# Performance work log

Measured on AMD Instinct MI355X. Metric: run time of the kernel, lower is better.

The kernel has to match this reference:

```python
import jax, jax.numpy as jnp
import numpy as np

B, S, D, H = 2, 2048, 512, 8
DK = D // H


def setup_inputs() -> dict:
    key = jax.random.key(0)
    ks = jax.random.split(key, 6)
    q = jax.random.normal(ks[0], (B, S, D), dtype=jnp.float32)
    k = jax.random.normal(ks[1], (B, S, D), dtype=jnp.float32)
    v = jax.random.normal(ks[2], (B, S, D), dtype=jnp.float32)
    mask = jax.random.randint(ks[3], (1, 1, S, S), 0, 2, dtype=jnp.int32)
    # nn.Linear weights [out, in]; scaled like torch default init
    Wq = jax.random.normal(ks[4], (D, D), dtype=jnp.float32) / np.sqrt(D)
    Wo = jax.random.normal(ks[5], (D, D), dtype=jnp.float32) / np.sqrt(D)
    return {"q": q, "k": k, "v": v, "mask": mask, "Wq": Wq, "Wo": Wo}


def _split_heads(x):
    # [B,S,D] -> [B,H,S,DK]
    return x.reshape(B, S, H, DK).transpose(0, 2, 1, 3)


def reference(q, k, v, mask, Wq, Wo):
    # NOTE: original module applies Wq to q, k AND v (faithful to source bug)
    query = _split_heads(q @ Wq.T)
    key_ = _split_heads(k @ Wq.T)
    value = _split_heads(v @ Wq.T)
    scores = jnp.einsum("bhqd,bhkd->bhqk", query, key_) / np.sqrt(DK).astype(np.float32)
    # original uses masked_fill_(mask==0, 1e-09) BEFORE softmax (not -inf)
    scores = jnp.where(mask == 0, jnp.float32(1e-9), scores)
    attn = jax.nn.softmax(scores, axis=-1)  # dropout p=0.0 -> identity
    x = jnp.einsum("bhqk,bhkd->bhqd", attn, value)
    x = x.transpose(0, 2, 1, 3).reshape(B, S, D)
    return x @ Wo.T
```

## Files before the change

kernel.cpp:

```cpp
#include <hip/hip_runtime.h>
#include <hip/hip_bf16.h>
#include <stdint.h>

#define S_LEN 2048
#define D_MOD 512
#define N_H   8
#define D_K   64

typedef short v8s __attribute__((ext_vector_type(8)));
typedef short v4s __attribute__((ext_vector_type(4)));
typedef float v4f __attribute__((ext_vector_type(4)));

__device__ __forceinline__ short f2bf(float f) {
  union { float f; unsigned u; } a; a.f = f;
  unsigned u = a.u;
  u += 0x7fffu + ((u >> 16) & 1u);
  return (short)(u >> 16);
}
__device__ __forceinline__ short f2bfh(float f) {
  union { float f; unsigned u; } a; a.f = f;
  return (short)((a.u + 0x8000u) >> 16);
}
__device__ __forceinline__ float bf2f(short s) {
  union { unsigned u; float f; } x;
  x.u = ((unsigned)(unsigned short)s) << 16;
  return x.f;
}

__device__ __forceinline__ v4f mfma16(v8s a, v8s b, v4f c) {
  return __builtin_amdgcn_mfma_f32_16x16x32_bf16(a, b, c, 0, 0, 0);
}
__device__ __forceinline__ v4f mfma16x16(v4s a, v4s b, v4f c) {
  return __builtin_amdgcn_mfma_f32_16x16x16bf16_1k(a, b, c, 0, 0, 0);
}

__global__ __launch_bounds__(256) void proj_kernel(
    const float* __restrict__ q, const float* __restrict__ k,
    const float* __restrict__ v, const float* __restrict__ Wq,
    const float* __restrict__ Wo, const int* __restrict__ mask,
    short* __restrict__ QP, short* __restrict__ KP, short* __restrict__ VT,
    short* __restrict__ Wob, unsigned long long* __restrict__ mp)
{
  const int z = blockIdx.z;
  const int tid = threadIdx.x;
  if (z == 3) {
    int bid = blockIdx.x * 8 + blockIdx.y;
    if (bid < 256) {
      int id = bid * 256 + tid;
      const int4* m4 = (const int4*)(mask + (size_t)id * 64);
      unsigned long long w = 0ull;
#pragma unroll
      for (int j = 0; j < 16; j++) {
        int4 mv = m4[j];
        w |= (unsigned long long)(mv.x != 0) << (j * 4 + 0);
        w |= (unsigned long long)(mv.y != 0) << (j * 4 + 1);
        w |= (unsigned long long)(mv.z != 0) << (j * 4 + 2);
        w |= (unsigned long long)(mv.w != 0) << (j * 4 + 3);
      }
      mp[id] = w;
    } else {
      unsigned off = (bid - 256) * 256 + tid;
      float4 x = ((const float4*)Wo)[off];
      v4s p; p.x = f2bf(x.x); p.y = f2bf(x.y); p.z = f2bf(x.z); p.w = f2bf(x.w);
      ((v4s*)Wob)[off] = p;
    }
    return;
  }
  const float* __restrict__ A = (z == 0) ? q : ((z == 1) ? k : v);
  const int m0 = blockIdx.x * 64, n0 = blockIdx.y * 64;
  const int wave = tid >> 6, lane = tid & 63;
  const int quad = lane >> 4, l15 = lane & 15;
  const int wm = wave >> 1, wn = wave & 1;
  __shared__ short As[64][72];
  __shared__ short Bs[64][72];
  v4f acc[2][2];
#pragma unroll
  for (int i = 0; i < 2; i++)
#pragma unroll
    for (int j = 0; j < 2; j++) acc[i][j] = (v4f){0.f, 0.f, 0.f, 0.f};

  float4 a4[4], b4[4];
#pragma unroll
  for (int i = 0; i < 4; i++) {
    int fi = tid + i * 256, r = fi >> 4, c = (fi & 15) << 2;
    a4[i] = *(const float4*)&A[(m0 + r) * 512 + c];
    b4[i] = *(const float4*)&Wq[(n0 + r) * 512 + c];
  }

  for (int kk = 0; kk < 512; kk += 64) {
    __syncthreads();
#pragma unroll
    for (int i = 0; i < 4; i++) {
      int fi = tid + i * 256, r = fi >> 4, c = (fi & 15) << 2;
      v4s ap; ap.x = f2bf(a4[i].x); ap.y = f2bf(a4[i].y); ap.z = f2bf(a4[i].z); ap.w = f2bf(a4[i].w);
      *(v4s*)&As[r][c] = ap;
      v4s bp; bp.x = f2bf(b4[i].x); bp.y = f2bf(b4[i].y); bp.z = f2bf(b4[i].z); bp.w = f2bf(b4[i].w);
      *(v4s*)&Bs[r][c] = bp;
    }
    __syncthreads();
    if (kk + 64 < 512) {
#pragma unroll
      for (int i = 0; i < 4; i++) {
        int fi = tid + i * 256, r = fi >> 4, c = (fi & 15) << 2;
        a4[i] = *(const float4*)&A[(m0 + r) * 512 + kk + 64 + c];
        b4[i] = *(const float4*)&Wq[(n0 + r) * 512 + kk + 64 + c];
      }
    }
#pragma unroll
    for (int ms = 0; ms < 2; ms++)
#pragma unroll
      for (int ns = 0; ns < 2; ns++)
#pragma unroll
        for (int ks = 0; ks < 2; ks++) {
          union { v8s v; v4s h2[2]; } a, bb;
          a.h2[0]  = *(const v4s*)&As[wm * 32 + ms * 16 + l15][ks * 32 + quad * 8];
          a.h2[1]  = *(const v4s*)&As[wm * 32 + ms * 16 + l15][ks * 32 + quad * 8 + 4];
          bb.h2[0] = *(const v4s*)&Bs[wn * 32 + ns * 16 + l15][ks * 32 + quad * 8];
          bb.h2[1] = *(const v4s*)&Bs[wn * 32 + ns * 16 + l15][ks * 32 + quad * 8 + 4];
          acc[ms][ns] = mfma16(a.v, bb.v, acc[ms][ns]);
        }
  }
#pragma unroll
  for (int ms = 0; ms < 2; ms++)
#pragma unroll
    for (int ns = 0; ns < 2; ns++) {
      int mb = m0 + wm * 32 + ms * 16 + quad * 4;
      int n  = n0 + wn * 32 + ns * 16 + l15;
      int bI = mb >> 11, s = mb & 2047, hh = n >> 6, dk = n & 63;
      if (z == 2) {
        v4s pv;
        pv.x = f2bf(acc[ms][ns][0]); pv.y = f2bf(acc[ms][ns][1]);
        pv.z = f2bf(acc[ms][ns][2]); pv.w = f2bf(acc[ms][ns][3]);
        *(v4s*)&VT[((bI * N_H + hh) * D_K + dk) * S_LEN + s] = pv;
      } else {
        short* dst = (z == 0) ? QP : KP;
#pragma unroll
        for (int r = 0; r < 4; r++)
          dst[((bI * N_H + hh) * S_LEN + (s + r)) * D_K + dk] = f2bf(acc[ms][ns][r]);
      }
    }
}

__global__ __launch_bounds__(512, 4) void attn_kernel(
    const short* __restrict__ QP, const short* __restrict__ KP,
    const short* __restrict__ VT, const unsigned long long* __restrict__ MP,
    short* __restrict__ XB)
{
  const int qt = blockIdx.x;
  const int h = blockIdx.y, b = blockIdx.z;
  const int tid = threadIdx.x;
  const int wave = tid >> 6, lane = tid & 63;
  const int quad = lane >> 4, l15 = lane & 15;
  const short* Qh = QP + ((b * N_H + h) * S_LEN) * D_K;
  const short* Kh = KP + ((b * N_H + h) * S_LEN) * D_K;
  const short* Vh = VT + ((b * N_H + h) * D_K) * S_LEN;

  __shared__ short Ks[2][64][72];
  __shared__ short Vs[2][64][72];

  const int qrow = qt * 128 + wave * 16;
  const int srow = tid >> 3;
  const int sc   = (tid & 7) * 8;

  v8s aQ[2];
#pragma unroll
  for (int ks = 0; ks < 2; ks++)
    aQ[ks] = *(const v8s*)&Qh[(qrow + l15) * D_K + ks * 32 + quad * 8];

  const float C1 = 0.18033688011112042f;
  const float C2 = -11.541560327111707f;
  const v4s ONES4 = {16256, 16256, 16256, 16256};
  v4f accX[4], accL = (v4f){0.f, 0.f, 0.f, 0.f};
#pragma unroll
  for (int u = 0; u < 4; u++) accX[u] = (v4f){0.f, 0.f, 0.f, 0.f};

  v8s kr = *(const v8s*)&Kh[srow * D_K + sc];
  v8s vr = *(const v8s*)&Vh[srow * S_LEN + sc];
  *(v8s*)&Ks[0][srow][sc] = kr;
  *(v8s*)&Vs[0][srow][sc] = vr;
  unsigned long long mwc = MP[(qrow + l15) * 32];
  unsigned long long mwn = 0ull;
  __syncthreads();

  for (int kt = 0; kt < 32; kt++) {
    const int cur = kt & 1;
    if (kt + 1 < 32) {
      const int c1 = (kt + 1) * 64;
      kr = *(const v8s*)&Kh[(c1 + srow) * D_K + sc];
      vr = *(const v8s*)&Vh[srow * S_LEN + c1 + sc];
      mwn = MP[(qrow + l15) * 32 + kt + 1];
    }

    v4s pa[4];
#pragma unroll
    for (int tp = 0; tp < 4; tp++) {
      v8s bK0 = *(const v8s*)&Ks[cur][tp * 16 + l15][quad * 8];
      v8s bK1 = *(const v8s*)&Ks[cur][tp * 16 + l15][32 + quad * 8];
      v4f s = mfma16(bK0, aQ[0], (v4f){0.f, 0.f, 0.f, 0.f});
      s = mfma16(bK1, aQ[1], s);
      unsigned mb = (unsigned)(mwc >> (tp * 16 + quad * 4));
      v4s pk;
#pragma unroll
      for (int r = 0; r < 4; r++) {
        float se = ((mb >> r) & 1u) ? s[r] : 0.0f;
        float p = __builtin_amdgcn_exp2f(fmaf(se, C1, C2));
        pk[r] = f2bfh(p);
      }
      pa[tp] = pk;
    }

#pragma unroll
    for (int u = 0; u < 4; u++) {
      const short* vb_ = &Vs[cur][u * 16 + l15][quad * 4];
#pragma unroll
      for (int tp = 0; tp < 4; tp++) {
        v4s bV = *(const v4s*)&vb_[tp * 16];
        accX[u] = mfma16x16(pa[tp], bV, accX[u]);
      }
    }
#pragma unroll
    for (int tp = 0; tp < 4; tp++)
      accL = mfma16x16(pa[tp], ONES4, accL);

    if (kt + 1 < 32) {
      *(v8s*)&Ks[cur ^ 1][srow][sc] = kr;
      *(v8s*)&Vs[cur ^ 1][srow][sc] = vr;
    }
    __syncthreads();
    mwc = mwn;
  }

  v4f linv;
#pragma unroll
  for (int r = 0; r < 4; r++) linv[r] = 1.0f / accL[r];
#pragma unroll
  for (int u = 0; u < 4; u++)
#pragma unroll
    for (int r = 0; r < 4; r++) {
      int srw = qrow + quad * 4 + r;
      XB[(b * S_LEN + srw) * D_MOD + h * D_K + u * 16 + l15] =
          f2bf(accX[u][r] * linv[r]);
    }
}

__global__ __launch_bounds__(256) void outproj_kernel(
    const short* __restrict__ XB, const short* __restrict__ Wob,
    float* __restrict__ out)
{
  const int m0 = blockIdx.x * 64, n0 = blockIdx.y * 64;
  const int tid = threadIdx.x;
  const int wave = tid >> 6, lane = tid & 63;
  const int quad = lane >> 4, l15 = lane & 15;
  const int wm = wave >> 1, wn = wave & 1;
  __shared__ short As[64][72];
  __shared__ short Bs[64][72];

  v4f acc[2][2];
#pragma unroll
  for (int i = 0; i < 2; i++)
#pragma unroll
    for (int j = 0; j < 2; j++) acc[i][j] = (v4f){0.f, 0.f, 0.f, 0.f};

  v8s a8[2], b8[2];
#pragma unroll
  for (int i = 0; i < 2; i++) {
    int fi = tid + i * 256, r = fi >> 3, c = (fi & 7) << 3;
    a8[i] = *(const v8s*)&XB[(m0 + r) * 512 + c];
    b8[i] = *(const v8s*)&Wob[(n0 + r) * 512 + c];
  }

  for (int kk = 0; kk < 512; kk += 64) {
    __syncthreads();
#pragma unroll
    for (int i = 0; i < 2; i++) {
      int fi = tid + i * 256, r = fi >> 3, c = (fi & 7) << 3;
      *(v8s*)&As[r][c] = a8[i];
      *(v8s*)&Bs[r][c] = b8[i];
    }
    __syncthreads();
    if (kk + 64 < 512) {
#pragma unroll
      for (int i = 0; i < 2; i++) {
        int fi = tid + i * 256, r = fi >> 3, c = (fi & 7) << 3;
        a8[i] = *(const v8s*)&XB[(m0 + r) * 512 + kk + 64 + c];
        b8[i] = *(const v8s*)&Wob[(n0 + r) * 512 + kk + 64 + c];
      }
    }
#pragma unroll
    for (int ms = 0; ms < 2; ms++)
#pragma unroll
      for (int ns = 0; ns < 2; ns++)
#pragma unroll
        for (int ks = 0; ks < 2; ks++) {
          union { v8s v; v4s h2[2]; } a, bb;
          a.h2[0]  = *(const v4s*)&As[wm * 32 + ms * 16 + l15][ks * 32 + quad * 8];
          a.h2[1]  = *(const v4s*)&As[wm * 32 + ms * 16 + l15][ks * 32 + quad * 8 + 4];
          bb.h2[0] = *(const v4s*)&Bs[wn * 32 + ns * 16 + l15][ks * 32 + quad * 8];
          bb.h2[1] = *(const v4s*)&Bs[wn * 32 + ns * 16 + l15][ks * 32 + quad * 8 + 4];
          acc[ms][ns] = mfma16(a.v, bb.v, acc[ms][ns]);
        }
  }
#pragma unroll
  for (int ms = 0; ms < 2; ms++)
#pragma unroll
    for (int ns = 0; ns < 2; ns++) {
      int n = n0 + wn * 32 + ns * 16 + l15;
#pragma unroll
      for (int r = 0; r < 4; r++) {
        int m = m0 + wm * 32 + ms * 16 + quad * 4 + r;
        out[m * 512 + n] = acc[ms][ns][r];
      }
    }
}

extern "C" void kernel_launch(void* const* d_in, const int* in_sizes, int n_in,
                              void* d_out, int out_size, void* d_ws, size_t ws_size,
                              hipStream_t stream) {
  const float* q  = (const float*)d_in[0];
  const float* k  = (const float*)d_in[1];
  const float* v  = (const float*)d_in[2];
  const int* mask = (const int*)d_in[3];
  const float* Wq = (const float*)d_in[4];
  const float* Wo = (const float*)d_in[5];
  float* out = (float*)d_out;
  char* ws = (char*)d_ws;
  short* QP = (short*)(ws);
  short* KP = (short*)(ws + (4u << 20));
  short* VT = (short*)(ws + (8u << 20));
  unsigned long long* MP = (unsigned long long*)(ws + (16u << 20));
  short* Wob = (short*)(ws + (16u << 20) + (512u << 10));
  short* XB = (short*)(ws + (17u << 20));

  proj_kernel<<<dim3(64, 8, 4), 256, 0, stream>>>(q, k, v, Wq, Wo, mask,
                                                  QP, KP, VT, Wob, MP);
  attn_kernel<<<dim3(16, N_H, 2), 512, 0, stream>>>(QP, KP, VT, MP, XB);
  outproj_kernel<<<dim3(64, 8, 1), 256, 0, stream>>>(XB, Wob, out);
}
```

Measured before the change: 163.3 us.

## Split attention key tiles across waves with swizzled LDS and cross-wave reduction

```diff
diff --git a/kernel.cpp b/kernel.cpp
--- a/kernel.cpp
+++ b/kernel.cpp
@@ -141,7 +141,7 @@
     }
 }
 
-__global__ __launch_bounds__(512, 4) void attn_kernel(
+__global__ __launch_bounds__(512, 8) void attn_kernel(
     const short* __restrict__ QP, const short* __restrict__ KP,
     const short* __restrict__ VT, const unsigned long long* __restrict__ MP,
     short* __restrict__ XB)
@@ -151,16 +151,18 @@
   const int tid = threadIdx.x;
   const int wave = tid >> 6, lane = tid & 63;
   const int quad = lane >> 4, l15 = lane & 15;
+  const int tp = wave & 3, qg = wave >> 2;
   const short* Qh = QP + ((b * N_H + h) * S_LEN) * D_K;
   const short* Kh = KP + ((b * N_H + h) * S_LEN) * D_K;
   const short* Vh = VT + ((b * N_H + h) * D_K) * S_LEN;
 
-  __shared__ short Ks[2][64][72];
-  __shared__ short Vs[2][64][72];
-
-  const int qrow = qt * 128 + wave * 16;
+  __shared__ short SMEM[2][2][64][64];
+
+  const int qrow = qt * 32 + qg * 16;
   const int srow = tid >> 3;
-  const int sc   = (tid & 7) * 8;
+  const int sc8  = (tid & 7) * 8;
+  const int scw  = sc8 ^ ((srow & 7) << 3);
+  const int swz  = (l15 & 7) << 3;
 
   v8s aQ[2];
 #pragma unroll
@@ -174,10 +176,10 @@
 #pragma unroll
   for (int u = 0; u < 4; u++) accX[u] = (v4f){0.f, 0.f, 0.f, 0.f};
 
-  v8s kr = *(const v8s*)&Kh[srow * D_K + sc];
-  v8s vr = *(const v8s*)&Vh[srow * S_LEN + sc];
-  *(v8s*)&Ks[0][srow][sc] = kr;
-  *(v8s*)&Vs[0][srow][sc] = vr;
+  v8s kr = *(const v8s*)&Kh[srow * D_K + sc8];
+  v8s vr = *(const v8s*)&Vh[srow * S_LEN + sc8];
+  *(v8s*)&SMEM[0][0][srow][scw] = kr;
+  *(v8s*)&SMEM[0][1][srow][scw] = vr;
   unsigned long long mwc = MP[(qrow + l15) * 32];
   unsigned long long mwn = 0ull;
   __syncthreads();
@@ -186,61 +188,67 @@
     const int cur = kt & 1;
     if (kt + 1 < 32) {
       const int c1 = (kt + 1) * 64;
-      kr = *(const v8s*)&Kh[(c1 + srow) * D_K + sc];
-      vr = *(const v8s*)&Vh[srow * S_LEN + c1 + sc];
+      kr = *(const v8s*)&Kh[(c1 + srow) * D_K + sc8];
+      vr = *(const v8s*)&Vh[srow * S_LEN + c1 + sc8];
       mwn = MP[(qrow + l15) * 32 + kt + 1];
     }
 
-    v4s pa[4];
-#pragma unroll
-    for (int tp = 0; tp < 4; tp++) {
-      v8s bK0 = *(const v8s*)&Ks[cur][tp * 16 + l15][quad * 8];
-      v8s bK1 = *(const v8s*)&Ks[cur][tp * 16 + l15][32 + quad * 8];
-      v4f s = mfma16(bK0, aQ[0], (v4f){0.f, 0.f, 0.f, 0.f});
-      s = mfma16(bK1, aQ[1], s);
-      unsigned mb = (unsigned)(mwc >> (tp * 16 + quad * 4));
-      v4s pk;
+    v8s bK0 = *(const v8s*)&SMEM[cur][0][tp * 16 + l15][(quad * 8) ^ swz];
+    v8s bK1 = *(const v8s*)&SMEM[cur][0][tp * 16 + l15][(32 + quad * 8) ^ swz];
+    v4f s = mfma16(bK0, aQ[0], (v4f){0.f, 0.f, 0.f, 0.f});
+    s = mfma16(bK1, aQ[1], s);
+    unsigned mb = (unsigned)(mwc >> (tp * 16 + quad * 4));
+    v4s pk;
+#pragma unroll
+    for (int r = 0; r < 4; r++) {
+      float se = ((mb >> r) & 1u) ? s[r] : 0.0f;
+      float p = __builtin_amdgcn_exp2f(fmaf(se, C1, C2));
+      pk[r] = f2bfh(p);
+    }
+
+#pragma unroll
+    for (int u = 0; u < 4; u++) {
+      v4s bV = *(const v4s*)&SMEM[cur][1][u * 16 + l15][(tp * 16 + quad * 4) ^ swz];
+      accX[u] = mfma16x16(pk, bV, accX[u]);
+    }
+    accL = mfma16x16(pk, ONES4, accL);
+
+    if (kt + 1 < 32) {
+      *(v8s*)&SMEM[cur ^ 1][0][srow][scw] = kr;
+      *(v8s*)&SMEM[cur ^ 1][1][srow][scw] = vr;
+    }
+    __syncthreads();
+    mwc = mwn;
+  }
+
+  v4f* ex4 = (v4f*)&SMEM[0][0][0][0];
+  if (tp != 0) {
+    int widx = (((tp - 1) * 2 + qg) * 64 + lane) * 5;
+#pragma unroll
+    for (int u = 0; u < 4; u++) ex4[widx + u] = accX[u];
+    ex4[widx + 4] = accL;
+  }
+  __syncthreads();
+  if (tp == 0) {
+#pragma unroll
+    for (int t2 = 1; t2 < 4; t2++) {
+      int widx = (((t2 - 1) * 2 + qg) * 64 + lane) * 5;
+#pragma unroll
+      for (int u = 0; u < 4; u++) accX[u] += ex4[widx + u];
+      accL += ex4[widx + 4];
+    }
+    v4f linv;
+#pragma unroll
+    for (int r = 0; r < 4; r++) linv[r] = 1.0f / accL[r];
+#pragma unroll
+    for (int u = 0; u < 4; u++)
 #pragma unroll
       for (int r = 0; r < 4; r++) {
-        float se = ((mb >> r) & 1u) ? s[r] : 0.0f;
-        float p = __builtin_amdgcn_exp2f(fmaf(se, C1, C2));
-        pk[r] = f2bfh(p);
-      }
-      pa[tp] = pk;
-    }
-
-#pragma unroll
-    for (int u = 0; u < 4; u++) {
-      const short* vb_ = &Vs[cur][u * 16 + l15][quad * 4];
-#pragma unroll
-      for (int tp = 0; tp < 4; tp++) {
-        v4s bV = *(const v4s*)&vb_[tp * 16];
-        accX[u] = mfma16x16(pa[tp], bV, accX[u]);
-      }
-    }
-#pragma unroll
-    for (int tp = 0; tp < 4; tp++)
-      accL = mfma16x16(pa[tp], ONES4, accL);
-
-    if (kt + 1 < 32) {
-      *(v8s*)&Ks[cur ^ 1][srow][sc] = kr;
-      *(v8s*)&Vs[cur ^ 1][srow][sc] = vr;
-    }
-    __syncthreads();
-    mwc = mwn;
-  }
-
-  v4f linv;
-#pragma unroll
-  for (int r = 0; r < 4; r++) linv[r] = 1.0f / accL[r];
-#pragma unroll
-  for (int u = 0; u < 4; u++)
-#pragma unroll
-    for (int r = 0; r < 4; r++) {
-      int srw = qrow + quad * 4 + r;
-      XB[(b * S_LEN + srw) * D_MOD + h * D_K + u * 16 + l15] =
-          f2bf(accX[u][r] * linv[r]);
-    }
+        int srw = qrow + quad * 4 + r;
+        XB[(b * S_LEN + srw) * D_MOD + h * D_K + u * 16 + l15] =
+            f2bf(accX[u][r] * linv[r]);
+      }
+  }
 }
 
 __global__ __launch_bounds__(256) void outproj_kernel(
@@ -333,6 +341,6 @@
 
   proj_kernel<<<dim3(64, 8, 4), 256, 0, stream>>>(q, k, v, Wq, Wo, mask,
                                                   QP, KP, VT, Wob, MP);
-  attn_kernel<<<dim3(16, N_H, 2), 512, 0, stream>>>(QP, KP, VT, MP, XB);
+  attn_kernel<<<dim3(64, N_H, 2), 512, 0, stream>>>(QP, KP, VT, MP, XB);
   outproj_kernel<<<dim3(64, 8, 1), 256, 0, stream>>>(XB, Wob, out);
 }
```

Result: slower. 166.8 us (+2.2%).

## Split attention key range across wave groups, swizzle LDS, use packed bf16 convert

Applied to the files above, without the earlier changes.

```diff
diff --git a/kernel.cpp b/kernel.cpp
--- a/kernel.cpp
+++ b/kernel.cpp
@@ -25,6 +25,11 @@
   union { unsigned u; float f; } x;
   x.u = ((unsigned)(unsigned short)s) << 16;
   return x.f;
+}
+__device__ __forceinline__ unsigned pk2(float a, float b) {
+  unsigned r;
+  asm("v_cvt_pk_bf16_f32 %0, %1, %2" : "=v"(r) : "v"(a), "v"(b));
+  return r;
 }
 
 __device__ __forceinline__ v4f mfma16(v8s a, v8s b, v4f c) {
@@ -92,10 +97,11 @@
 #pragma unroll
     for (int i = 0; i < 4; i++) {
       int fi = tid + i * 256, r = fi >> 4, c = (fi & 15) << 2;
-      v4s ap; ap.x = f2bf(a4[i].x); ap.y = f2bf(a4[i].y); ap.z = f2bf(a4[i].z); ap.w = f2bf(a4[i].w);
-      *(v4s*)&As[r][c] = ap;
-      v4s bp; bp.x = f2bf(b4[i].x); bp.y = f2bf(b4[i].y); bp.z = f2bf(b4[i].z); bp.w = f2bf(b4[i].w);
-      *(v4s*)&Bs[r][c] = bp;
+      union { unsigned u[2]; v4s s; } ap, bp;
+      ap.u[0] = pk2(a4[i].x, a4[i].y); ap.u[1] = pk2(a4[i].z, a4[i].w);
+      bp.u[0] = pk2(b4[i].x, b4[i].y); bp.u[1] = pk2(b4[i].z, b4[i].w);
+      *(v4s*)&As[r][c] = ap.s;
+      *(v4s*)&Bs[r][c] = bp.s;
     }
     __syncthreads();
     if (kk + 64 < 512) {
@@ -144,23 +150,25 @@
 __global__ __launch_bounds__(512, 4) void attn_kernel(
     const short* __restrict__ QP, const short* __restrict__ KP,
     const short* __restrict__ VT, const unsigned long long* __restrict__ MP,
-    short* __restrict__ XB)
+    short* __restrict__ X)
 {
   const int qt = blockIdx.x;
   const int h = blockIdx.y, b = blockIdx.z;
   const int tid = threadIdx.x;
   const int wave = tid >> 6, lane = tid & 63;
   const int quad = lane >> 4, l15 = lane & 15;
+  const int qw = wave & 3, kg = wave >> 2;
   const short* Qh = QP + ((b * N_H + h) * S_LEN) * D_K;
   const short* Kh = KP + ((b * N_H + h) * S_LEN) * D_K;
   const short* Vh = VT + ((b * N_H + h) * D_K) * S_LEN;
 
-  __shared__ short Ks[2][64][72];
-  __shared__ short Vs[2][64][72];
-
-  const int qrow = qt * 128 + wave * 16;
+  __shared__ short SMEM[2][2][2][64][64];
+
+  const int qrow = qt * 64 + qw * 16;
   const int srow = tid >> 3;
-  const int sc   = (tid & 7) * 8;
+  const int sc8  = (tid & 7) * 8;
+  const int scw  = sc8 ^ ((srow & 7) << 3);
+  const int swz  = (l15 & 7) << 3;
 
   v8s aQ[2];
 #pragma unroll
@@ -174,28 +182,34 @@
 #pragma unroll
   for (int u = 0; u < 4; u++) accX[u] = (v4f){0.f, 0.f, 0.f, 0.f};
 
-  v8s kr = *(const v8s*)&Kh[srow * D_K + sc];
-  v8s vr = *(const v8s*)&Vh[srow * S_LEN + sc];
-  *(v8s*)&Ks[0][srow][sc] = kr;
-  *(v8s*)&Vs[0][srow][sc] = vr;
-  unsigned long long mwc = MP[(qrow + l15) * 32];
+  v8s kr0 = *(const v8s*)&Kh[srow * D_K + sc8];
+  v8s vr0 = *(const v8s*)&Vh[srow * S_LEN + sc8];
+  v8s kr1 = *(const v8s*)&Kh[(64 + srow) * D_K + sc8];
+  v8s vr1 = *(const v8s*)&Vh[srow * S_LEN + 64 + sc8];
+  *(v8s*)&SMEM[0][0][0][srow][scw] = kr0;
+  *(v8s*)&SMEM[0][0][1][srow][scw] = vr0;
+  *(v8s*)&SMEM[0][1][0][srow][scw] = kr1;
+  *(v8s*)&SMEM[0][1][1][srow][scw] = vr1;
+  unsigned long long mwc = MP[(qrow + l15) * 32 + kg];
   unsigned long long mwn = 0ull;
   __syncthreads();
 
-  for (int kt = 0; kt < 32; kt++) {
-    const int cur = kt & 1;
-    if (kt + 1 < 32) {
-      const int c1 = (kt + 1) * 64;
-      kr = *(const v8s*)&Kh[(c1 + srow) * D_K + sc];
-      vr = *(const v8s*)&Vh[srow * S_LEN + c1 + sc];
-      mwn = MP[(qrow + l15) * 32 + kt + 1];
+  for (int it = 0; it < 16; it++) {
+    const int p = it & 1;
+    if (it + 1 < 16) {
+      const int c0 = (it + 1) * 128, c1 = c0 + 64;
+      kr0 = *(const v8s*)&Kh[(c0 + srow) * D_K + sc8];
+      vr0 = *(const v8s*)&Vh[srow * S_LEN + c0 + sc8];
+      kr1 = *(const v8s*)&Kh[(c1 + srow) * D_K + sc8];
+      vr1 = *(const v8s*)&Vh[srow * S_LEN + c1 + sc8];
+      mwn = MP[(qrow + l15) * 32 + 2 * (it + 1) + kg];
     }
 
     v4s pa[4];
 #pragma unroll
     for (int tp = 0; tp < 4; tp++) {
-      v8s bK0 = *(const v8s*)&Ks[cur][tp * 16 + l15][quad * 8];
-      v8s bK1 = *(const v8s*)&Ks[cur][tp * 16 + l15][32 + quad * 8];
+      v8s bK0 = *(const v8s*)&SMEM[p][kg][0][tp * 16 + l15][(quad * 8) ^ swz];
+      v8s bK1 = *(const v8s*)&SMEM[p][kg][0][tp * 16 + l15][(32 + quad * 8) ^ swz];
       v4f s = mfma16(bK0, aQ[0], (v4f){0.f, 0.f, 0.f, 0.f});
       s = mfma16(bK1, aQ[1], s);
       unsigned mb = (unsigned)(mwc >> (tp * 16 + quad * 4));
@@ -203,18 +217,18 @@
 #pragma unroll
       for (int r = 0; r < 4; r++) {
         float se = ((mb >> r) & 1u) ? s[r] : 0.0f;
-        float p = __builtin_amdgcn_exp2f(fmaf(se, C1, C2));
-        pk[r] = f2bfh(p);
+        float pr = __builtin_amdgcn_exp2f(fmaf(se, C1, C2));
+        pk[r] = f2bfh(pr);
       }
       pa[tp] = pk;
     }
 
 #pragma unroll
     for (int u = 0; u < 4; u++) {
-      const short* vb_ = &Vs[cur][u * 16 + l15][quad * 4];
+      const short* vb_ = &SMEM[p][kg][1][u * 16 + l15][0];
 #pragma unroll
       for (int tp = 0; tp < 4; tp++) {
-        v4s bV = *(const v4s*)&vb_[tp * 16];
+        v4s bV = *(const v4s*)&vb_[(tp * 16 + quad * 4) ^ swz];
         accX[u] = mfma16x16(pa[tp], bV, accX[u]);
       }
     }
@@ -222,29 +236,50 @@
     for (int tp = 0; tp < 4; tp++)
       accL = mfma16x16(pa[tp], ONES4, accL);
 
-    if (kt + 1 < 32) {
-      *(v8s*)&Ks[cur ^ 1][srow][sc] = kr;
-      *(v8s*)&Vs[cur ^ 1][srow][sc] = vr;
+    if (it + 1 < 16) {
+      *(v8s*)&SMEM[p ^ 1][0][0][srow][scw] = kr0;
+      *(v8s*)&SMEM[p ^ 1][0][1][srow][scw] = vr0;
+      *(v8s*)&SMEM[p ^ 1][1][0][srow][scw] = kr1;
+      *(v8s*)&SMEM[p ^ 1][1][1][srow][scw] = vr1;
     }
     __syncthreads();
     mwc = mwn;
   }
 
-  v4f linv;
-#pragma unroll
-  for (int r = 0; r < 4; r++) linv[r] = 1.0f / accL[r];
-#pragma unroll
-  for (int u = 0; u < 4; u++)
-#pragma unroll
-    for (int r = 0; r < 4; r++) {
-      int srw = qrow + quad * 4 + r;
-      XB[(b * S_LEN + srw) * D_MOD + h * D_K + u * 16 + l15] =
-          f2bf(accX[u][r] * linv[r]);
-    }
+  float* ex = (float*)&SMEM[0][0][0][0][0];
+  const int xi = (qw * 64 + lane) * 21;
+  if (kg == 1) {
+#pragma unroll
+    for (int u = 0; u < 4; u++)
+#pragma unroll
+      for (int r = 0; r < 4; r++) ex[xi + u * 4 + r] = accX[u][r];
+#pragma unroll
+    for (int r = 0; r < 4; r++) ex[xi + 16 + r] = accL[r];
+  }
+  __syncthreads();
+  if (kg == 0) {
+#pragma unroll
+    for (int u = 0; u < 4; u++)
+#pragma unroll
+      for (int r = 0; r < 4; r++) accX[u][r] += ex[xi + u * 4 + r];
+#pragma unroll
+    for (int r = 0; r < 4; r++) accL[r] += ex[xi + 16 + r];
+    v4f linv;
+#pragma unroll
+    for (int r = 0; r < 4; r++) linv[r] = 1.0f / accL[r];
+#pragma unroll
+    for (int u = 0; u < 4; u++)
+#pragma unroll
+      for (int r = 0; r < 4; r++) {
+        int srw = qrow + quad * 4 + r;
+        X[(b * S_LEN + srw) * D_MOD + h * D_K + u * 16 + l15] =
+            f2bf(accX[u][r] * linv[r]);
+      }
+  }
 }
 
 __global__ __launch_bounds__(256) void outproj_kernel(
-    const short* __restrict__ XB, const short* __restrict__ Wob,
+    const short* __restrict__ X, const short* __restrict__ Wob,
     float* __restrict__ out)
 {
   const int m0 = blockIdx.x * 64, n0 = blockIdx.y * 64;
@@ -265,7 +300,7 @@
 #pragma unroll
   for (int i = 0; i < 2; i++) {
     int fi = tid + i * 256, r = fi >> 3, c = (fi & 7) << 3;
-    a8[i] = *(const v8s*)&XB[(m0 + r) * 512 + c];
+    a8[i] = *(const v8s*)&X[(m0 + r) * 512 + c];
     b8[i] = *(const v8s*)&Wob[(n0 + r) * 512 + c];
   }
 
@@ -282,7 +317,7 @@
 #pragma unroll
       for (int i = 0; i < 2; i++) {
         int fi = tid + i * 256, r = fi >> 3, c = (fi & 7) << 3;
-        a8[i] = *(const v8s*)&XB[(m0 + r) * 512 + kk + 64 + c];
+        a8[i] = *(const v8s*)&X[(m0 + r) * 512 + kk + 64 + c];
         b8[i] = *(const v8s*)&Wob[(n0 + r) * 512 + kk + 64 + c];
       }
     }
@@ -329,10 +364,10 @@
   short* VT = (short*)(ws + (8u << 20));
   unsigned long long* MP = (unsigned long long*)(ws + (16u << 20));
   short* Wob = (short*)(ws + (16u << 20) + (512u << 10));
-  short* XB = (short*)(ws + (17u << 20));
+  short* X  = (short*)(ws + (17u << 20));
 
   proj_kernel<<<dim3(64, 8, 4), 256, 0, stream>>>(q, k, v, Wq, Wo, mask,
                                                   QP, KP, VT, Wob, MP);
-  attn_kernel<<<dim3(16, N_H, 2), 512, 0, stream>>>(QP, KP, VT, MP, XB);
-  outproj_kernel<<<dim3(64, 8, 1), 256, 0, stream>>>(XB, Wob, out);
-}
+  attn_kernel<<<dim3(32, N_H, 2), 512, 0, stream>>>(QP, KP, VT, MP, X);
+  outproj_kernel<<<dim3(64, 8, 1), 256, 0, stream>>>(X, Wob, out);
+}
```

New measurement: 148.2 us. -9.3%, faster.
